# Performance work log

Hardware: AMD Instinct MI355X
Metric: run time of the kernel (lower is better)

Reference implementation:

```python
import jax, jax.numpy as jnp
import numpy as np


def setup_inputs() -> dict:
    key = jax.random.key(0)
    k1, k2 = jax.random.split(key)
    B, D = 1048576, 16
    model_out = jax.random.normal(k1, (B, D), dtype=jnp.float32)
    y_true = jax.random.normal(k2, (B, D), dtype=jnp.float32)
    return {"model_out": model_out, "y_true": y_true}


def _elem_loss(x, y):
    # nn.MSELoss(reduction='none'): elementwise squared error
    return (x - y) ** 2


def reference(model_out, y_true):
    # loss: [B, D] elementwise
    loss = _elem_loss(model_out, y_true)

    # d_loss = d(loss.sum())/d(model_out), same shape as model_out
    d_loss = jax.grad(lambda x: _elem_loss(x, y_true).sum())(model_out)

    # sqd_loss[b, i, j] = d^2 loss / d x[b,i] d x[b,j].
    # Loss is elementwise (no cross-batch coupling), so the Hessian is
    # block-diagonal over batch: compute a [D, D] per-sample Hessian via
    # vmap(jacfwd(grad)) instead of the torch per-dim autograd loop.
    def per_sample_grad(x_b, y_b):  # [D] -> [D]
        return jax.grad(lambda x: _elem_loss(x, y_b).sum())(x_b)

    sqd_loss = jax.vmap(
        lambda x_b, y_b: jax.jacfwd(per_sample_grad)(x_b, y_b)
    )(model_out, y_true)  # [B, D, D]

    return loss, d_loss, sqd_loss
```

## Files before the change

kernel.cpp:

```cpp
#include <hip/hip_runtime.h>


typedef float v4f __attribute__((ext_vector_type(4)));

__global__ __launch_bounds__(256) void fused_loss_hess(
    const v4f* __restrict__ x,
    const v4f* __restrict__ y,
    v4f* __restrict__ loss,
    v4f* __restrict__ dloss,
    v4f* __restrict__ sqd,
    unsigned int n4_ld,
    unsigned int n4_h) {
    const unsigned int T   = gridDim.x * blockDim.x;
    const unsigned int tid = blockIdx.x * blockDim.x + threadIdx.x;

    for (unsigned int i = tid; i < n4_ld; i += T) {
        v4f a = x[i];
        v4f b = y[i];
        v4f d = a - b;
        loss[i]  = d * d;
        dloss[i] = d + d;
    }

    {
        const unsigned int f   = tid << 2;
        const unsigned int col = f & 15u;
        const unsigned int row = (f >> 4) & 15u;
        v4f v;
        v.x = (row == col)      ? 2.0f : 0.0f;
        v.y = (row == col + 1u) ? 2.0f : 0.0f;
        v.z = (row == col + 2u) ? 2.0f : 0.0f;
        v.w = (row == col + 3u) ? 2.0f : 0.0f;
#pragma unroll 8
        for (unsigned int i = tid; i < n4_h; i += T) {
            sqd[i] = v;
        }
    }
}

extern "C" void kernel_launch(void* const* d_in, const int* in_sizes, int n_in,
                              void* d_out, int out_size, void* d_ws, size_t ws_size,
                              hipStream_t stream) {
    const float* model_out = (const float*)d_in[0];
    const float* y_true    = (const float*)d_in[1];
    float* out = (float*)d_out;

    const int BD = in_sizes[0];
    float* loss_p  = out;
    float* dloss_p = out + BD;
    float* sqd_p   = out + 2 * (size_t)BD;

    const unsigned int n4_ld = (unsigned int)(BD / 4);
    const unsigned int n4_h  = (unsigned int)((size_t)BD * 16 / 4);

    const int block = 256;
    const int grid  = 2048;
    fused_loss_hess<<<grid, block, 0, stream>>>(
        (const v4f*)model_out, (const v4f*)y_true,
        (v4f*)loss_p, (v4f*)dloss_p, (v4f*)sqd_p,
        n4_ld, n4_h);
}
```

Before: 1.290 ms.

## Split loss/grad and Hessian fill into separate kernels with per-wave contiguous chunks

Moves the elementwise loss and gradient into a one-element-per-thread kernel. The 1 GiB Hessian fill goes to a separate kernel in which each wavefront writes one contiguous chunk with four unrolled stores per iteration, instead of grid-stride interleaving. This aims to improve write streaming and DRAM page locality for the write-bound fill. It adds a second launch, plus a fallback fill kernel for sizes that don't divide evenly.

```diff
diff --git a/kernel.cpp b/kernel.cpp
--- a/kernel.cpp
+++ b/kernel.cpp
@@ -3,39 +3,60 @@
 
 typedef float v4f __attribute__((ext_vector_type(4)));
 
-__global__ __launch_bounds__(256) void fused_loss_hess(
+__global__ __launch_bounds__(256) void loss_grad_kernel(
     const v4f* __restrict__ x,
     const v4f* __restrict__ y,
     v4f* __restrict__ loss,
     v4f* __restrict__ dloss,
-    v4f* __restrict__ sqd,
-    unsigned int n4_ld,
-    unsigned int n4_h) {
-    const unsigned int T   = gridDim.x * blockDim.x;
-    const unsigned int tid = blockIdx.x * blockDim.x + threadIdx.x;
+    int n4) {
+    int i = blockIdx.x * blockDim.x + threadIdx.x;
+    if (i >= n4) return;
+    v4f a = x[i];
+    v4f b = y[i];
+    v4f d = a - b;
+    loss[i]  = d * d;
+    dloss[i] = d + d;
+}
 
-    for (unsigned int i = tid; i < n4_ld; i += T) {
-        v4f a = x[i];
-        v4f b = y[i];
-        v4f d = a - b;
-        loss[i]  = d * d;
-        dloss[i] = d + d;
+__global__ __launch_bounds__(256) void hess_stream_fill(
+    v4f* __restrict__ out, unsigned int chunk ) {
+    const unsigned int lane = threadIdx.x & 63u;
+    const unsigned int wpb  = blockDim.x >> 6;
+    const unsigned int wid  = blockIdx.x * wpb + (threadIdx.x >> 6);
+
+    const unsigned int f   = lane << 2;
+    const unsigned int col = f & 15u;
+    const unsigned int row = (f >> 4) & 15u;
+    v4f v;
+    v.x = (row == col)      ? 2.0f : 0.0f;
+    v.y = (row == col + 1u) ? 2.0f : 0.0f;
+    v.z = (row == col + 2u) ? 2.0f : 0.0f;
+    v.w = (row == col + 3u) ? 2.0f : 0.0f;
+
+    v4f* p = out + (size_t)wid * chunk + lane;
+    const unsigned int iters = chunk >> 8;
+    for (unsigned int it = 0; it < iters; ++it) {
+        p[0]   = v;
+        p[64]  = v;
+        p[128] = v;
+        p[192] = v;
+        p += 256;
     }
+}
 
-    {
-        const unsigned int f   = tid << 2;
-        const unsigned int col = f & 15u;
-        const unsigned int row = (f >> 4) & 15u;
-        v4f v;
-        v.x = (row == col)      ? 2.0f : 0.0f;
-        v.y = (row == col + 1u) ? 2.0f : 0.0f;
-        v.z = (row == col + 2u) ? 2.0f : 0.0f;
-        v.w = (row == col + 3u) ? 2.0f : 0.0f;
-#pragma unroll 8
-        for (unsigned int i = tid; i < n4_h; i += T) {
-            sqd[i] = v;
-        }
-    }
+__global__ __launch_bounds__(256) void hess_fill_kernel(
+    v4f* __restrict__ out, unsigned int n4) {
+    unsigned int i = blockIdx.x * blockDim.x + threadIdx.x;
+    if (i >= n4) return;
+    unsigned int ff  = i << 2;
+    unsigned int col = ff & 15u;
+    unsigned int row = (ff >> 4) & 15u;
+    v4f v;
+    v.x = (row == col)      ? 2.0f : 0.0f;
+    v.y = (row == col + 1u) ? 2.0f : 0.0f;
+    v.z = (row == col + 2u) ? 2.0f : 0.0f;
+    v.w = (row == col + 3u) ? 2.0f : 0.0f;
+    out[i] = v;
 }
 
 extern "C" void kernel_launch(void* const* d_in, const int* in_sizes, int n_in,
@@ -50,13 +71,26 @@
     float* dloss_p = out + BD;
     float* sqd_p   = out + 2 * (size_t)BD;
 
-    const unsigned int n4_ld = (unsigned int)(BD / 4);
-    const unsigned int n4_h  = (unsigned int)((size_t)BD * 16 / 4);
+    {
+        int n4 = BD / 4;
+        int block = 256;
+        int grid = (n4 + block - 1) / block;
+        loss_grad_kernel<<<grid, block, 0, stream>>>(
+            (const v4f*)model_out, (const v4f*)y_true,
+            (v4f*)loss_p, (v4f*)dloss_p, n4);
+    }
 
-    const int block = 256;
-    const int grid  = 2048;
-    fused_loss_hess<<<grid, block, 0, stream>>>(
-        (const v4f*)model_out, (const v4f*)y_true,
-        (v4f*)loss_p, (v4f*)dloss_p, (v4f*)sqd_p,
-        n4_ld, n4_h);
+    {
+        unsigned int n4 = (unsigned int)((size_t)BD * 16 / 4);
+        const int block  = 256;
+        const int grid   = 1024;
+        const unsigned int nw = (unsigned int)grid * (block / 64);
+        if (n4 % (nw * 256u) == 0u) {
+            unsigned int chunk = n4 / nw;
+            hess_stream_fill<<<grid, block, 0, stream>>>((v4f*)sqd_p, chunk);
+        } else {
+            unsigned int g = (n4 + block - 1) / block;
+            hess_fill_kernel<<<g, block, 0, stream>>>((v4f*)sqd_p, n4);
+        }
+    }
 }
```

After: 1.269 ms. Within noise of the previous version (-1.6%).
